# Kernel tuning notes

Measured on AMD Instinct MI355X. Metric: run time of the kernel, lower is better.

Reference implementation:

```python
import jax, jax.numpy as jnp
import numpy as np

INPUT_DIM = 1024
LATENT_DIM = 16 * INPUT_DIM
K_VALUES = (32, 128, 256)


def setup_inputs() -> dict:
    key = jax.random.key(0)
    ks = jax.random.split(key, 7)
    B = 4096
    x = jax.random.normal(ks[0], (B, INPUT_DIM), dtype=jnp.float32)
    MLP_output = jax.random.normal(ks[1], (B, INPUT_DIM), dtype=jnp.float32)
    # encoder: nn.Linear(input_dim, latent_dim) -> weight [latent, input], bias zeroed in __init__
    W_enc = jax.random.normal(ks[2], (LATENT_DIM, INPUT_DIM), dtype=jnp.float32) / np.sqrt(INPUT_DIM)
    b_enc = jnp.zeros((LATENT_DIM,), dtype=jnp.float32)
    # decoder / skip / b_dec are zeros in __init__, but use small random values so the
    # reference exercises non-trivial math (zeros would make decode degenerate)
    W_dec = jax.random.normal(ks[3], (LATENT_DIM, INPUT_DIM), dtype=jnp.float32) * 0.02
    b_dec = jax.random.normal(ks[4], (INPUT_DIM,), dtype=jnp.float32) * 0.02
    W_skip = jax.random.normal(ks[5], (INPUT_DIM, INPUT_DIM), dtype=jnp.float32) * 0.02
    return {"x": x, "MLP_output": MLP_output, "W_enc": W_enc, "b_enc": b_enc,
            "W_dec": W_dec, "b_dec": b_dec, "W_skip": W_skip}


def _topk_relu(z, k):
    # keep top-k per row, relu the kept values, zero elsewhere (scatter)
    vals, idx = jax.lax.top_k(z, k)                     # [B, k]
    vals = jax.nn.relu(vals)
    rows = jnp.arange(z.shape[0])[:, None]              # [B, 1]
    return jnp.zeros_like(z).at[rows, idx].set(vals)


def reference(x, MLP_output, W_enc, b_enc, W_dec, b_dec, W_skip):
    B = x.shape[0]
    pre = x @ W_enc.T + b_enc                            # [B, latent] (shared across k)
    skip = x @ W_skip + b_dec                            # [B, input]
    total_variance = jnp.sum((x - x.mean(0)) ** 2)

    mean_encoded = jnp.zeros((B, LATENT_DIM), dtype=x.dtype)
    mean_decoded = jnp.zeros((B, INPUT_DIM), dtype=x.dtype)
    total_loss = jnp.asarray(0.0, dtype=x.dtype)
    encoded = None
    for k in K_VALUES:                                   # fixed small set of k values
        encoded = _topk_relu(pre, k)                     # [B, latent]
        decoded = encoded @ W_dec + skip                 # [B, input]
        mean_encoded = mean_encoded + encoded
        mean_decoded = mean_decoded + decoded
        total_loss = total_loss + jnp.sum((MLP_output - decoded) ** 2)

    n = float(len(K_VALUES))
    mean_encoded = mean_encoded / n
    mean_decoded = mean_decoded / n
    total_loss = total_loss / total_variance
    # l0 over the last (k=256) encoded tensor
    l0_norm_final = jnp.sum(jnp.count_nonzero(encoded, axis=0))
    return (mean_encoded, mean_decoded, total_loss, l0_norm_final)
```

## Files before the change

### kernel.cpp

```cpp
#include <hip/hip_runtime.h>
#include <stdint.h>

typedef short   bf16x8 __attribute__((ext_vector_type(8)));
typedef float   f32x4  __attribute__((ext_vector_type(4)));
typedef float   f32x16 __attribute__((ext_vector_type(16)));
typedef int     i32x4  __attribute__((ext_vector_type(4)));
typedef int     i32x8  __attribute__((ext_vector_type(8)));
typedef unsigned short u16x8 __attribute__((ext_vector_type(8)));
typedef unsigned long long u64;
typedef long long i64;
typedef long long i64x2 __attribute__((ext_vector_type(2)));

#define B_ROWS 4096
#define D_IN   1024
#define L_DIM  16384
#define NBIN   2048
#define CCAP   1024
#define SLOTS  32
#define W8SCALE 1200.0f

__device__ __forceinline__ unsigned short f2bf(float f) {
  unsigned int u = __float_as_uint(f);
  u = (u + 0x7FFFu + ((u >> 16) & 1u)) >> 16;
  return (unsigned short)u;
}
__device__ __forceinline__ float bf2f(unsigned short h) {
  return __uint_as_float(((unsigned int)h) << 16);
}
__device__ __forceinline__ unsigned char f2e4m3(float v) {
  unsigned int u = __float_as_uint(v);
  unsigned int s = (u >> 24) & 0x80u;
  unsigned int a = u & 0x7FFFFFFFu;
  unsigned int r = (a + 0x0007FFFFu + ((a >> 20) & 1u)) >> 20;
  if (r <= (120u << 3)) return (unsigned char)s;
  r -= (120u << 3);
  if (r > 0x7Eu) r = 0x7Eu;
  return (unsigned char)(s | r);
}
__device__ __forceinline__ float e4m3f(unsigned char b) {
  unsigned int e = (b >> 3) & 0xFu, m = b & 7u, s = ((unsigned int)b & 0x80u) << 24;
  if (e == 0) return __uint_as_float(s);
  return __uint_as_float(s | ((e + 120u) << 23) | (m << 20));
}
__device__ __forceinline__ unsigned int sortkey(float f) {
  unsigned int u = __float_as_uint(f);
  return (u & 0x80000000u) ? ~u : (u | 0x80000000u);
}
__device__ __forceinline__ float keyval(unsigned int k) {
  unsigned int u = (k & 0x80000000u) ? (k & 0x7FFFFFFFu) : ~k;
  return __uint_as_float(u);
}
__device__ __forceinline__ int binof(float v) {
  int b = (int)((v + 2.0f) * (2048.0f / 7.0f));
  return b < 0 ? 0 : (b > 2047 ? 2047 : b);
}
__device__ __forceinline__ void gl_lds16(const void* g, void* l) {
  __builtin_amdgcn_global_load_lds(
      (const __attribute__((address_space(1))) unsigned int*)g,
      (__attribute__((address_space(3))) unsigned int*)l, 16, 0, 0);
}
__device__ __forceinline__ float waveSum(float v) {
  #pragma unroll
  for (int m = 32; m; m >>= 1) v += __shfl_xor(v, m);
  return v;
}

__global__ void k_prep(const float* __restrict__ x,
                       unsigned short* __restrict__ xb, unsigned char* __restrict__ xf8,
                       float* scal, float* colsum, float* colsq, unsigned int* rowcnt,
                       int n4) {
  int gt = blockIdx.x * blockDim.x + threadIdx.x;
  if (gt < 8) scal[gt] = 0.f;
  if (gt < 1024) { colsum[gt] = 0.f; colsq[gt] = 0.f; }
  if (gt < B_ROWS) rowcnt[gt] = 0u;
  int stride = gridDim.x * blockDim.x;
  for (int i = gt; i < n4; i += stride) {
    f32x4 v = *((const f32x4*)x + i);
    ushort4 o;
    o.x = f2bf(v[0]); o.y = f2bf(v[1]); o.z = f2bf(v[2]); o.w = f2bf(v[3]);
    *((ushort4*)xb + i) = o;
    unsigned int u = 0;
    #pragma unroll
    for (int j = 0; j < 4; j++) u |= ((unsigned int)f2e4m3(v[j])) << (8 * j);
    *((unsigned int*)xf8 + i) = u;
  }
}

__global__ void k_convert_fp8(const float* __restrict__ in, unsigned char* __restrict__ out, int n4) {
  int i = blockIdx.x * blockDim.x + threadIdx.x;
  int stride = gridDim.x * blockDim.x;
  for (; i < n4; i += stride) {
    f32x4 v = *((const f32x4*)in + i);
    unsigned int u = 0;
    #pragma unroll
    for (int j = 0; j < 4; j++) u |= ((unsigned int)f2e4m3(v[j])) << (8 * j);
    *((unsigned int*)out + i) = u;
  }
}

__global__ void k_convert_i8(const float* __restrict__ in, unsigned int* __restrict__ out, int n4) {
  int i = blockIdx.x * blockDim.x + threadIdx.x;
  int stride = gridDim.x * blockDim.x;
  for (; i < n4; i += stride) {
    f32x4 v = *((const f32x4*)in + i);
    unsigned int u = 0;
    #pragma unroll
    for (int j = 0; j < 4; j++) {
      int q = (int)rintf(v[j] * W8SCALE);
      q = q > 127 ? 127 : (q < -127 ? -127 : q);
      u |= ((unsigned int)q & 0xFFu) << (8 * j);
    }
    out[i] = u;
  }
}

__global__ void k_transpose_bf(const float* __restrict__ in, unsigned short* __restrict__ out, int n) {
  __shared__ float tile[32][33];
  int bx = blockIdx.x * 32, by = blockIdx.y * 32;
  int tx = threadIdx.x, ty = threadIdx.y;
  tile[ty][tx] = in[(size_t)(by + ty) * n + bx + tx];
  __syncthreads();
  out[(size_t)(bx + ty) * n + by + tx] = f2bf(tile[tx][ty]);
}

__global__ __launch_bounds__(256) void k_var1(const float* __restrict__ x, float* colsum, float* colsq) {
  int g = blockIdx.x;
  int t = threadIdx.x;
  float s[4] = {0,0,0,0}, q[4] = {0,0,0,0};
  for (int r = 0; r < 32; r++) {
    const float* rp = x + (size_t)(g * 32 + r) * D_IN;
    #pragma unroll
    for (int j = 0; j < 4; j++) {
      float v = rp[t + 256 * j];
      s[j] += v; q[j] += v * v;
    }
  }
  #pragma unroll
  for (int j = 0; j < 4; j++) {
    atomicAdd(&colsum[t + 256 * j], s[j]);
    atomicAdd(&colsq [t + 256 * j], q[j]);
  }
}

__global__ __launch_bounds__(256) void k_var2(const float* colsum, const float* colsq, float* scal) {
  __shared__ float red[4];
  int t = threadIdx.x;
  float loc = 0.f;
  #pragma unroll
  for (int j = 0; j < 4; j++) {
    int c = t + 256 * j;
    float cs = colsum[c], cq = colsq[c];
    loc += cq - cs * cs * (1.f / (float)B_ROWS);
  }
  loc = waveSum(loc);
  if ((t & 63) == 0) red[t >> 6] = loc;
  __syncthreads();
  if (t == 0) scal[1] = red[0] + red[1] + red[2] + red[3];
}

__device__ __forceinline__ void stage_half8(const unsigned char* __restrict__ G,
                                            int Kb, int r0, int k0b,
                                            unsigned char* buf, int t) {
  #pragma unroll
  for (int j = 0; j < 2; j++) {
    int q = j * 256 + t;
    int row = q >> 2, u = q & 3;
    int uu = u ^ ((row >> 1) & 3);
    gl_lds16(&G[(size_t)(r0 + row) * Kb + k0b + uu * 16], &buf[q * 16]);
  }
}

__global__ __launch_bounds__(256, 3) void k_gemm_enc(
    const unsigned char* __restrict__ A8, const unsigned char* __restrict__ B8,
    const float* __restrict__ bias,
    u64* __restrict__ cand, unsigned int* __restrict__ rowcnt,
    int M, int N, int K) {
  __shared__ unsigned char sBuf[3 * 16384];
  unsigned int*  stageKey = (unsigned int*)sBuf;
  unsigned char* stageCol = (unsigned char*)&sBuf[16384];
  unsigned int*  s_cnt    = (unsigned int*)&sBuf[20480];
  unsigned int*  s_base   = (unsigned int*)&sBuf[21504];

  const int t = threadIdx.x;
  const int w = t >> 6, l = t & 63;
  const int wr = w >> 1, wc = w & 1;
  const int lr = l & 31, lh = l >> 5;
  const int row0 = blockIdx.y * 128, col0 = blockIdx.x * 128;
  const int Kb = K;
  const int NT = K >> 6;

  f32x16 acc[2][2] = {};

  stage_half8(A8, Kb, row0, 0,   sBuf + 0,             t);
  stage_half8(B8, Kb, col0, 0,   sBuf + 8192,          t);
  stage_half8(A8, Kb, row0, 64,  sBuf + 16384,         t);
  stage_half8(B8, Kb, col0, 64,  sBuf + 16384 + 8192,  t);

  const int raf = wr * 64 + lr,  swa = (raf >> 1) & 3;
  const int rbf = wc * 64 + lr,  swb = (rbf >> 1) & 3;
  const int uA0 = ((2 * lh)     ^ swa) * 16, uA1 = ((2 * lh + 1) ^ swa) * 16;
  const int uB0 = ((2 * lh)     ^ swb) * 16, uB1 = ((2 * lh + 1) ^ swb) * 16;
  const int offA0 = raf * 64,        offA1 = (raf + 32) * 64;
  const int offB0 = 8192 + rbf * 64, offB1 = 8192 + (rbf + 32) * 64;

  for (int tt = 0; tt < NT; tt++) {
    asm volatile("s_waitcnt vmcnt(4)" ::: "memory");
    __builtin_amdgcn_s_barrier();

    int ks = (tt + 2 < NT) ? (tt + 2) : (NT - 1);
    unsigned char* nb = sBuf + ((tt + 2) % 3) * 16384;
    stage_half8(A8, Kb, row0, ks * 64, nb, t);
    stage_half8(B8, Kb, col0, ks * 64, nb + 8192, t);

    const unsigned char* cb = sBuf + (tt % 3) * 16384;

    union Frag { i32x8 w; i32x4 h[2]; };
    Frag av[2], bv[2];
    av[0].h[0] = *(const i32x4*)&cb[offA0 + uA0];
    av[0].h[1] = *(const i32x4*)&cb[offA0 + uA1];
    av[1].h[0] = *(const i32x4*)&cb[offA1 + uA0];
    av[1].h[1] = *(const i32x4*)&cb[offA1 + uA1];
    bv[0].h[0] = *(const i32x4*)&cb[offB0 + uB0];
    bv[0].h[1] = *(const i32x4*)&cb[offB0 + uB1];
    bv[1].h[0] = *(const i32x4*)&cb[offB1 + uB0];
    bv[1].h[1] = *(const i32x4*)&cb[offB1 + uB1];

    __builtin_amdgcn_s_setprio(1);
    #pragma unroll
    for (int mt = 0; mt < 2; mt++)
      #pragma unroll
      for (int nt = 0; nt < 2; nt++)
        acc[mt][nt] = __builtin_amdgcn_mfma_scale_f32_32x32x64_f8f6f4(
            av[mt].w, bv[nt].w, acc[mt][nt],
            0, 0,
            0, 0x7F7F7F7Fu,
            0, 0x7F7F7F7Fu);
    __builtin_amdgcn_s_setprio(0);
  }

  asm volatile("s_waitcnt vmcnt(0) lgkmcnt(0)" ::: "memory");
  __syncthreads();

  if (t < 128) s_cnt[t] = 0u;
  __syncthreads();

  #pragma unroll
  for (int nt = 0; nt < 2; nt++) {
    int cl = wc * 64 + nt * 32 + lr;
    float bvs = bias[col0 + cl];
    #pragma unroll
    for (int mt = 0; mt < 2; mt++) {
      int rbase = wr * 64 + mt * 32 + lh * 4;
      #pragma unroll
      for (int i = 0; i < 16; i++) {
        float v = acc[mt][nt][i] + bvs;
        if (v > 1.7f) {
          int r = rbase + (i & 3) + 8 * (i >> 2);
          unsigned int p = atomicAdd(&s_cnt[r], 1u);
          if (p < SLOTS) {
            stageKey[r * SLOTS + p] = sortkey(v);
            stageCol[r * SLOTS + p] = (unsigned char)cl;
          }
        }
      }
    }
  }
  __syncthreads();

  if (t < 128) {
    unsigned int c = s_cnt[t];
    if (c > SLOTS)      { atomicAdd(&rowcnt[row0 + t], 4096u); s_base[t] = 0x80000000u; }
    else if (c)         s_base[t] = atomicAdd(&rowcnt[row0 + t], c);
    else                s_base[t] = 0u;
  }
  __syncthreads();

  for (int s = t; s < 128 * SLOTS; s += 256) {
    int r = s >> 5, p = s & (SLOTS - 1);
    unsigned int c = s_cnt[r], g0 = s_base[r];
    if ((unsigned int)p < c && c <= SLOTS && !(g0 & 0x80000000u)) {
      unsigned int g = g0 + (unsigned int)p;
      if (g < CCAP)
        cand[(size_t)(row0 + r) * CCAP + g] =
            ((u64)stageKey[s] << 32) | (unsigned int)(~(unsigned int)(col0 + stageCol[s]));
    }
  }
}

__device__ __forceinline__ void stage_swz(const unsigned short* __restrict__ G, int ld,
                                          int r0, int k0, unsigned short* lds, int t) {
  #pragma unroll
  for (int j = 0; j < 4; j++) {
    int q = j * 256 + t;
    int row = q >> 3, u = q & 7;
    int uu = u ^ (row & 7);
    gl_lds16(&G[(size_t)(r0 + row) * ld + k0 + uu * 8], &lds[q * 8]);
  }
}

__device__ __forceinline__ void gemm_core(
    const unsigned short* __restrict__ A, const unsigned short* __restrict__ Bm,
    unsigned short* sA, unsigned short* sB,
    int row0, int col0, int K, int t, int wr, int wc, int lm, int u0,
    f32x4 acc[4][4]) {
  for (int k0 = 0; k0 < K; k0 += 64) {
    stage_swz(A,  K, row0, k0, sA, t);
    stage_swz(Bm, K, col0, k0, sB, t);
    __syncthreads();
    bf16x8 af[4][2], bfr[4][2];
    #pragma unroll
    for (int i = 0; i < 4; i++) {
      int r = wr * 64 + i * 16 + lm;
      int sw = r & 7;
      af[i][0] = *(const bf16x8*)&sA[r * 64 + ((u0 ^ sw) * 8)];
      af[i][1] = *(const bf16x8*)&sA[r * 64 + (((u0 + 4) ^ sw) * 8)];
    }
    #pragma unroll
    for (int n = 0; n < 4; n++) {
      int r = wc * 64 + n * 16 + lm;
      int sw = r & 7;
      bfr[n][0] = *(const bf16x8*)&sB[r * 64 + ((u0 ^ sw) * 8)];
      bfr[n][1] = *(const bf16x8*)&sB[r * 64 + (((u0 + 4) ^ sw) * 8)];
    }
    #pragma unroll
    for (int i = 0; i < 4; i++)
      #pragma unroll
      for (int n = 0; n < 4; n++) {
        acc[i][n] = __builtin_amdgcn_mfma_f32_16x16x32_bf16(af[i][0], bfr[n][0], acc[i][n], 0, 0, 0);
        acc[i][n] = __builtin_amdgcn_mfma_f32_16x16x32_bf16(af[i][1], bfr[n][1], acc[i][n], 0, 0, 0);
      }
    __syncthreads();
  }
}

__global__ __launch_bounds__(256) void k_gemm_skip(
    const unsigned short* __restrict__ A, const unsigned short* __restrict__ Bm,
    const float* __restrict__ bias, unsigned short* __restrict__ Cb,
    int M, int N, int K) {
  __shared__ unsigned short sA[128 * 64];
  __shared__ unsigned short sB[128 * 64];
  const int t = threadIdx.x;
  const int w = t >> 6, l = t & 63;
  const int wr = w >> 1, wc = w & 1;
  const int lm = l & 15, u0 = l >> 4;
  const int row0 = blockIdx.y * 128, col0 = blockIdx.x * 128;

  f32x4 acc[4][4] = {};
  gemm_core(A, Bm, sA, sB, row0, col0, K, t, wr, wc, lm, u0, acc);

  const int lg = l >> 4;
  #pragma unroll
  for (int n = 0; n < 4; n++) {
    int col = col0 + wc * 64 + n * 16 + lm;
    float bv = bias[col];
    #pragma unroll
    for (int i = 0; i < 4; i++) {
      int rbase = row0 + wr * 64 + i * 16 + lg * 4;
      #pragma unroll
      for (int j = 0; j < 4; j++)
        Cb[(size_t)(rbase + j) * N + col] = f2bf(acc[i][n][j] + bv);
    }
  }
}

__global__ __launch_bounds__(256) void k_select(
    const u64* __restrict__ cand, const unsigned int* __restrict__ rowcnt,
    const unsigned char* __restrict__ xf8, const unsigned char* __restrict__ wenc8,
    const float* __restrict__ benc,
    float* __restrict__ menc, uint2* __restrict__ lists, unsigned int* __restrict__ l0p) {
  __shared__ u64 sc[CCAP];
  __shared__ unsigned int hist[NBIN];
  __shared__ u64 scratch[256];
  __shared__ unsigned int sS[256];
  __shared__ uint2 win[256];
  __shared__ int s_bb[3];
  __shared__ unsigned int s_bc[3];
  __shared__ u64 s_T[3];
  __shared__ int s_scnt;
  __shared__ unsigned int s_l0, s_pos;

  const int b = blockIdx.x, t = threadIdx.x;
  float* rowp = menc + (size_t)b * L_DIM;

  int cnt = (int)rowcnt[b];
  if (cnt >= 256 && cnt <= CCAP) {
    for (int i = t; i < cnt; i += 256) sc[i] = cand[(size_t)b * CCAP + i];
    #pragma unroll 4
    for (int g = 0; g < 16; g++) {
      f32x4 z = {};
      *(f32x4*)&rowp[g * 1024 + t * 4] = z;
    }
    __syncthreads();
  } else {
    unsigned char* xrow = (unsigned char*)scratch;
    for (int i = t; i < D_IN; i += 256) xrow[i] = xf8[(size_t)b * D_IN + i];
    __syncthreads();
    for (int q = 0; q < 64; q++) {
      int lat = q * 256 + t;
      const unsigned char* wp = &wenc8[(size_t)lat * D_IN];
      float a = 0.f;
      for (int k = 0; k < D_IN; k++) a += e4m3f(xrow[k]) * e4m3f(wp[k]);
      rowp[lat] = a + benc[lat];
    }
    __syncthreads();
    float T = 1.7f;
    for (int at = 0; at < 10; at++) {
      if (t == 0) s_scnt = 0;
      __syncthreads();
      int loc = 0;
      for (int q = 0; q < 64; q++) loc += (rowp[q * 256 + t] > T) ? 1 : 0;
      atomicAdd(&s_scnt, loc);
      __syncthreads();
      int c2 = s_scnt;
      if (c2 >= 256 && c2 <= CCAP) break;
      T = (c2 < 256) ? (T - 0.5f) : (T + 0.3f);
      __syncthreads();
    }
    if (t == 0) s_scnt = 0;
    __syncthreads();
    for (int q = 0; q < 64; q++) {
      int lat = q * 256 + t;
      float v = rowp[lat];
      if (v > T) {
        int p = atomicAdd(&s_scnt, 1);
        if (p < CCAP) sc[p] = ((u64)sortkey(v) << 32) | (unsigned int)(~(unsigned int)lat);
      }
    }
    __syncthreads();
    cnt = min(s_scnt, CCAP);
    for (int i = t * 4; i < L_DIM; i += 1024) { f32x4 z = {}; *(f32x4*)&rowp[i] = z; }
    __syncthreads();
  }

  for (int i = t; i < NBIN; i += 256) hist[i] = 0u;
  __syncthreads();
  for (int i = t; i < cnt; i += 256) {
    float v = keyval((unsigned int)(sc[i] >> 32));
    atomicAdd(&hist[binof(v)], 1u);
  }
  __syncthreads();

  unsigned int csum = 0;
  #pragma unroll
  for (int j = 0; j < 8; j++) csum += hist[t * 8 + j];
  sS[t] = csum;
  __syncthreads();
  for (int off = 1; off < 256; off <<= 1) {
    unsigned int v2 = (t + off < 256) ? sS[t + off] : 0u;
    __syncthreads();
    sS[t] += v2;
    __syncthreads();
  }
  {
    unsigned int above = (t < 255) ? sS[t + 1] : 0u;
    unsigned int run = 0;
    for (int j = 7; j >= 0; j--) {
      int bb = t * 8 + j;
      unsigned int S = above + run, h = hist[bb];
      if (h) {
        if (S < 32u  && 32u  <= S + h) { s_bb[0] = bb; s_bc[0] = S; }
        if (S < 128u && 128u <= S + h) { s_bb[1] = bb; s_bc[1] = S; }
        if (S < 256u && 256u <= S + h) { s_bb[2] = bb; s_bc[2] = S; }
      }
      run += h;
    }
  }
  __syncthreads();

  for (int ri = 0; ri < 3; ri++) {
    const int r = (ri == 0) ? 32 : (ri == 1) ? 128 : 256;
    int bb = s_bb[ri];
    int cA = (int)s_bc[ri];
    if (t == 0) s_scnt = 0;
    __syncthreads();
    for (int i = t; i < cnt; i += 256) {
      float v = keyval((unsigned int)(sc[i] >> 32));
      if (binof(v) == bb) {
        int p = atomicAdd(&s_scnt, 1);
        if (p < 256) scratch[p] = sc[i];
      }
    }
    __syncthreads();
    int m = min(s_scnt, 256);
    for (int i = t; i < m; i += 256) {
      u64 me = scratch[i];
      int rk = 0;
      for (int j2 = 0; j2 < m; j2++) rk += (scratch[j2] > me) ? 1 : 0;
      if (rk == r - cA - 1) s_T[ri] = me;
    }
    __syncthreads();
  }

  if (t == 0) { s_pos = 0u; s_l0 = 0u; }
  __syncthreads();
  const u64 T32 = s_T[0], T128 = s_T[1], T256 = s_T[2];
  for (int i = t; i < cnt; i += 256) {
    u64 e = sc[i];
    int w = (e >= T32) ? 3 : (e >= T128) ? 2 : (e >= T256) ? 1 : 0;
    if (w) {
      unsigned int p = atomicAdd(&s_pos, 1u);
      int idx = (int)(~(unsigned int)e) & (L_DIM - 1);
      float v = keyval((unsigned int)(e >> 32));
      float rv = fmaxf(v, 0.f);
      if (p < 256u)
        win[p] = make_uint2((unsigned int)idx | ((unsigned int)w << 20), __float_as_uint(rv));
      if (rv > 0.f) atomicAdd(&s_l0, 1u);
    }
  }
  __syncthreads();
  for (int i = (int)s_pos + t; i < 256; i += 256) win[i] = make_uint2(0xFFFFFu, 0u);
  __syncthreads();

  for (int k = 2; k <= 256; k <<= 1) {
    for (int j = k >> 1; j > 0; j >>= 1) {
      int x = t ^ j;
      if (x > t) {
        uint2 a = win[t], bb2 = win[x];
        bool asc = ((t & k) == 0);
        bool swap = asc ? ((a.x & 0xFFFFFu) > (bb2.x & 0xFFFFFu))
                        : ((a.x & 0xFFFFFu) < (bb2.x & 0xFFFFFu));
        if (swap) { win[t] = bb2; win[x] = a; }
      }
      __syncthreads();
    }
  }

  lists[(size_t)b * 256 + t] = win[t];

  {
    uint2 e = win[t];
    int idx = (int)(e.x & 0xFFFFFu) & (L_DIM - 1);
    unsigned int wg = (e.x >> 20) & 3u;
    float rv = __uint_as_float(e.y);
    rowp[idx] = rv * (float)wg * (1.f / 3.f);
  }

  if (t == 0) atomicAdd(l0p, s_l0);
}

#define DEC_PROC(E, Q)                                             \
  do {                                                             \
    int wgt_ = (int)(((E).x >> 20) & 3u);                          \
    float v_ = __uint_as_float((E).y) * (1.0f / W8SCALE);          \
    float f_[8];                                                   \
    _Pragma("unroll")                                              \
    for (int j_ = 0; j_ < 4; j_++) {                               \
      f_[j_]     = (float)((int)((Q).x << (24 - 8 * j_)) >> 24);   \
      f_[4 + j_] = (float)((int)((Q).y << (24 - 8 * j_)) >> 24);   \
    }                                                              \
    if (wgt_ == 3) {                                               \
      _Pragma("unroll")                                            \
      for (int j_ = 0; j_ < 8; j_++) a1[j_] += v_ * f_[j_];        \
    } else if (wgt_ == 2) {                                        \
      _Pragma("unroll")                                            \
      for (int j_ = 0; j_ < 8; j_++) a2[j_] += v_ * f_[j_];        \
    } else {                                                       \
      _Pragma("unroll")                                            \
      for (int j_ = 0; j_ < 8; j_++) a3[j_] += v_ * f_[j_];        \
    }                                                              \
  } while (0)

__global__ __launch_bounds__(512) void k_decode(
    const uint2* __restrict__ lists, const unsigned char* __restrict__ W8,
    const unsigned short* __restrict__ skipb, const float* __restrict__ mlp,
    float* __restrict__ mdec, float* __restrict__ loss_acc) {
  __shared__ uint2 ll[256];
  __shared__ float part[3][24][128];
  __shared__ float red[2];
  const int b = blockIdx.x, t = threadIdx.x;
  if (t < 256) ll[t] = lists[(size_t)b * 256 + t];
  __syncthreads();

  const int lane = t & 127, grp = t >> 7;
  const int c = lane * 8;

  float a1[8] = {}, a2[8] = {}, a3[8] = {};

  for (int i0 = 0; i0 < 64; i0 += 8) {
    uint2 e0 = ll[4 * (i0 + 0) + grp];
    uint2 e1 = ll[4 * (i0 + 1) + grp];
    uint2 e2 = ll[4 * (i0 + 2) + grp];
    uint2 e3 = ll[4 * (i0 + 3) + grp];
    uint2 e4 = ll[4 * (i0 + 4) + grp];
    uint2 e5 = ll[4 * (i0 + 5) + grp];
    uint2 e6 = ll[4 * (i0 + 6) + grp];
    uint2 e7 = ll[4 * (i0 + 7) + grp];
    const unsigned char* r0p = W8 + (size_t)((unsigned)__builtin_amdgcn_readfirstlane(e0.x) & (L_DIM - 1)) * D_IN;
    const unsigned char* r1p = W8 + (size_t)((unsigned)__builtin_amdgcn_readfirstlane(e1.x) & (L_DIM - 1)) * D_IN;
    const unsigned char* r2p = W8 + (size_t)((unsigned)__builtin_amdgcn_readfirstlane(e2.x) & (L_DIM - 1)) * D_IN;
    const unsigned char* r3p = W8 + (size_t)((unsigned)__builtin_amdgcn_readfirstlane(e3.x) & (L_DIM - 1)) * D_IN;
    const unsigned char* r4p = W8 + (size_t)((unsigned)__builtin_amdgcn_readfirstlane(e4.x) & (L_DIM - 1)) * D_IN;
    const unsigned char* r5p = W8 + (size_t)((unsigned)__builtin_amdgcn_readfirstlane(e5.x) & (L_DIM - 1)) * D_IN;
    const unsigned char* r6p = W8 + (size_t)((unsigned)__builtin_amdgcn_readfirstlane(e6.x) & (L_DIM - 1)) * D_IN;
    const unsigned char* r7p = W8 + (size_t)((unsigned)__builtin_amdgcn_readfirstlane(e7.x) & (L_DIM - 1)) * D_IN;
    uint2 q0 = *(const uint2*)(r0p + c);
    uint2 q1 = *(const uint2*)(r1p + c);
    uint2 q2 = *(const uint2*)(r2p + c);
    uint2 q3 = *(const uint2*)(r3p + c);
    uint2 q4 = *(const uint2*)(r4p + c);
    uint2 q5 = *(const uint2*)(r5p + c);
    uint2 q6 = *(const uint2*)(r6p + c);
    uint2 q7 = *(const uint2*)(r7p + c);
    DEC_PROC(e0, q0);
    DEC_PROC(e1, q1);
    DEC_PROC(e2, q2);
    DEC_PROC(e3, q3);
    DEC_PROC(e4, q4);
    DEC_PROC(e5, q5);
    DEC_PROC(e6, q6);
    DEC_PROC(e7, q7);
  }

  if (grp != 0) {
    #pragma unroll
    for (int j = 0; j < 8; j++) {
      part[grp - 1][j][lane]      = a1[j];
      part[grp - 1][8 + j][lane]  = a2[j];
      part[grp - 1][16 + j][lane] = a3[j];
    }
  }
  __syncthreads();

  float lsum = 0.f;
  if (grp == 0) {
    #pragma unroll
    for (int g = 0; g < 3; g++) {
      #pragma unroll
      for (int j = 0; j < 8; j++) {
        a1[j] += part[g][j][lane];
        a2[j] += part[g][8 + j][lane];
        a3[j] += part[g][16 + j][lane];
      }
    }
    u16x8 skv = *(const u16x8*)&skipb[(size_t)b * D_IN + c];
    f32x4 m0 = *(const f32x4*)&mlp[(size_t)b * D_IN + c];
    f32x4 m1 = *(const f32x4*)&mlp[(size_t)b * D_IN + c + 4];
    float mm[8] = {m0[0], m0[1], m0[2], m0[3], m1[0], m1[1], m1[2], m1[3]};
    float md[8];
    #pragma unroll
    for (int j = 0; j < 8; j++) {
      float sk   = bf2f(skv[j]);
      float d32  = sk + a1[j];
      float d128 = d32 + a2[j];
      float d256 = d128 + a3[j];
      md[j] = (d32 + d128 + d256) * (1.f / 3.f);
      float e1 = mm[j] - d32, e2 = mm[j] - d128, e3 = mm[j] - d256;
      lsum += e1 * e1 + e2 * e2 + e3 * e3;
    }
    f32x4 o0 = {md[0], md[1], md[2], md[3]};
    f32x4 o1 = {md[4], md[5], md[6], md[7]};
    *(f32x4*)&mdec[(size_t)b * D_IN + c]     = o0;
    *(f32x4*)&mdec[(size_t)b * D_IN + c + 4] = o1;
  }

  lsum = waveSum(lsum);
  if ((t & 63) == 0 && t < 128) red[t >> 6] = lsum;
  __syncthreads();
  if (t == 0) atomicAdd(loss_acc, red[0] + red[1]);
}

__global__ void k_final(const float* scal, const unsigned int* l0p, float* outscal) {
  outscal[0] = scal[0] / scal[1];
  outscal[1] = (float)(*l0p);
}

extern "C" void kernel_launch(void* const* d_in, const int* in_sizes, int n_in,
                              void* d_out, int out_size, void* d_ws, size_t ws_size,
                              hipStream_t stream) {
  (void)in_sizes; (void)n_in; (void)out_size; (void)ws_size;
  const float* x     = (const float*)d_in[0];
  const float* mlp   = (const float*)d_in[1];
  const float* Wenc  = (const float*)d_in[2];
  const float* benc  = (const float*)d_in[3];
  const float* Wdec  = (const float*)d_in[4];
  const float* bdec  = (const float*)d_in[5];
  const float* Wskip = (const float*)d_in[6];

  char* ws = (char*)d_ws;
  float*          scal    = (float*)(ws + 0);
  unsigned int*   l0p     = (unsigned int*)(ws + 8);
  float*          colsum  = (float*)(ws + 256);
  float*          colsq   = (float*)(ws + 4352);
  unsigned int*   rowcnt  = (unsigned int*)(ws + 8448);
  unsigned short* xb      = (unsigned short*)(ws + 24832);
  unsigned char*  wenc8   = (unsigned char*)(ws + 8413440);
  unsigned char*  xf8     = (unsigned char*)(ws + 8413440 + 16777216);
  unsigned short* wsktb   = (unsigned short*)(ws + 41967872);
  unsigned short* skipb   = (unsigned short*)(ws + 44065024);
  uint2*          lists   = (uint2*)(ws + 52453632);
  u64*            cand    = (u64*)(ws + 60842240);
  unsigned char*  wdec8   = (unsigned char*)(ws + 60842240);

  float* out  = (float*)d_out;
  float* menc = out;
  float* mdec = out + (size_t)B_ROWS * L_DIM;
  float* oscl = out + (size_t)B_ROWS * L_DIM + (size_t)B_ROWS * D_IN;

  k_prep<<<2048, 256, 0, stream>>>(x, xb, xf8, scal, colsum, colsq, rowcnt, (B_ROWS * D_IN) / 4);
  k_convert_fp8<<<2048, 256, 0, stream>>>(Wenc, wenc8, (L_DIM * D_IN) / 4);
  k_transpose_bf<<<dim3(32, 32), dim3(32, 32), 0, stream>>>(Wskip, wsktb, D_IN);
  k_var1<<<128, 256, 0, stream>>>(x, colsum, colsq);
  k_var2<<<1, 256, 0, stream>>>(colsum, colsq, scal);
  k_gemm_enc<<<dim3(L_DIM / 128, B_ROWS / 128), 256, 0, stream>>>(
      xf8, wenc8, benc, cand, rowcnt, B_ROWS, L_DIM, D_IN);
  k_gemm_skip<<<dim3(D_IN / 128, B_ROWS / 128), 256, 0, stream>>>(
      xb, wsktb, bdec, skipb, B_ROWS, D_IN, D_IN);
  k_select<<<B_ROWS, 256, 0, stream>>>(cand, rowcnt, xf8, wenc8, benc, menc, lists, l0p);
  k_convert_i8<<<2048, 256, 0, stream>>>(Wdec, (unsigned int*)wdec8, (L_DIM * D_IN) / 4);
  k_decode<<<B_ROWS, 512, 0, stream>>>(lists, wdec8, skipb, mlp, mdec, scal);
  k_final<<<1, 1, 0, stream>>>(scal, l0p, oscl);
}
```

Baseline: 456.9 us.

## Triple-buffer skip GEMM shared memory with async prefetch two tiles ahead

Replaces the synchronous load-sync-compute-sync loop of the skip GEMM with a three-stage LDS ring buffer. Global-to-LDS copies for tile tt+2 are issued before computing tile tt, and the wait is a partial vmcnt plus a single barrier per iteration. MFMA sections are wrapped in s_setprio. The aim is to hide global load latency behind matrix math. In exchange the kernel uses 96KB of LDS, which lowers occupancy, and depends on hand-placed waitcnt correctness. Only the small skip GEMM (K=1024) is affected, so the end-to-end impact is limited.

```diff
diff --git a/kernel.cpp b/kernel.cpp
--- a/kernel.cpp
+++ b/kernel.cpp
@@ -298,15 +298,37 @@
   }
 }
 
-__device__ __forceinline__ void gemm_core(
+__global__ __launch_bounds__(256) void k_gemm_skip(
     const unsigned short* __restrict__ A, const unsigned short* __restrict__ Bm,
-    unsigned short* sA, unsigned short* sB,
-    int row0, int col0, int K, int t, int wr, int wc, int lm, int u0,
-    f32x4 acc[4][4]) {
-  for (int k0 = 0; k0 < K; k0 += 64) {
-    stage_swz(A,  K, row0, k0, sA, t);
-    stage_swz(Bm, K, col0, k0, sB, t);
-    __syncthreads();
+    const float* __restrict__ bias, unsigned short* __restrict__ Cb,
+    int M, int N, int K) {
+  __shared__ unsigned short sBuf[3 * 16384];
+  const int t = threadIdx.x;
+  const int w = t >> 6, l = t & 63;
+  const int wr = w >> 1, wc = w & 1;
+  const int lm = l & 15, u0 = l >> 4;
+  const int row0 = blockIdx.y * 128, col0 = blockIdx.x * 128;
+  const int NT = K >> 6;
+
+  f32x4 acc[4][4] = {};
+
+  stage_swz(A,  K, row0, 0,  sBuf + 0,            t);
+  stage_swz(Bm, K, col0, 0,  sBuf + 8192,         t);
+  stage_swz(A,  K, row0, 64, sBuf + 16384,        t);
+  stage_swz(Bm, K, col0, 64, sBuf + 16384 + 8192, t);
+
+  for (int tt = 0; tt < NT; tt++) {
+    asm volatile("s_waitcnt vmcnt(8)" ::: "memory");
+    __builtin_amdgcn_s_barrier();
+
+    int ks = (tt + 2 < NT) ? (tt + 2) : (NT - 1);
+    unsigned short* nb = sBuf + ((tt + 2) % 3) * 16384;
+    stage_swz(A,  K, row0, ks * 64, nb, t);
+    stage_swz(Bm, K, col0, ks * 64, nb + 8192, t);
+
+    const unsigned short* sA = sBuf + (tt % 3) * 16384;
+    const unsigned short* sB = sA + 8192;
+
     bf16x8 af[4][2], bfr[4][2];
     #pragma unroll
     for (int i = 0; i < 4; i++) {
@@ -322,6 +344,7 @@
       bfr[n][0] = *(const bf16x8*)&sB[r * 64 + ((u0 ^ sw) * 8)];
       bfr[n][1] = *(const bf16x8*)&sB[r * 64 + (((u0 + 4) ^ sw) * 8)];
     }
+    __builtin_amdgcn_s_setprio(1);
     #pragma unroll
     for (int i = 0; i < 4; i++)
       #pragma unroll
@@ -329,24 +352,10 @@
         acc[i][n] = __builtin_amdgcn_mfma_f32_16x16x32_bf16(af[i][0], bfr[n][0], acc[i][n], 0, 0, 0);
         acc[i][n] = __builtin_amdgcn_mfma_f32_16x16x32_bf16(af[i][1], bfr[n][1], acc[i][n], 0, 0, 0);
       }
-    __syncthreads();
-  }
-}
-
-__global__ __launch_bounds__(256) void k_gemm_skip(
-    const unsigned short* __restrict__ A, const unsigned short* __restrict__ Bm,
-    const float* __restrict__ bias, unsigned short* __restrict__ Cb,
-    int M, int N, int K) {
-  __shared__ unsigned short sA[128 * 64];
-  __shared__ unsigned short sB[128 * 64];
-  const int t = threadIdx.x;
-  const int w = t >> 6, l = t & 63;
-  const int wr = w >> 1, wc = w & 1;
-  const int lm = l & 15, u0 = l >> 4;
-  const int row0 = blockIdx.y * 128, col0 = blockIdx.x * 128;
-
-  f32x4 acc[4][4] = {};
-  gemm_core(A, Bm, sA, sB, row0, col0, K, t, wr, wc, lm, u0, acc);
+    __builtin_amdgcn_s_setprio(0);
+  }
+
+  asm volatile("s_waitcnt vmcnt(0) lgkmcnt(0)" ::: "memory");
 
   const int lg = l >> 4;
   #pragma unroll
```

New measurement: 449.7 us, median of 2. Within noise of the previous version (-1.6%).
